# Kernel tuning notes

Hardware: AMD Instinct MI355X
Metric: run time of the kernel (lower is better)

## Reference

```python
import jax, jax.numpy as jnp
import numpy as np
from jax import lax

B, T, QD, ED, AD = 256, 512, 1024, 512, 128
NF, KS = 32, 31  # location filters, kernel size
PAD = (KS - 1) // 2


def setup_inputs() -> dict:
    key = jax.random.key(0)
    ks = jax.random.split(key, 12)
    query = jax.random.normal(ks[0], (B, QD), jnp.float32)
    inputs = jax.random.normal(ks[1], (B, T, ED), jnp.float32)
    processed_inputs = jax.random.normal(ks[2], (B, T, AD), jnp.float32)
    mask = jnp.ones((B, T), jnp.bool_)
    # init_states()
    attention_weights = jnp.zeros((B, T), jnp.float32)
    attention_weights_cum = jnp.zeros((B, T), jnp.float32)
    alpha = jnp.concatenate([jnp.ones((B, 1)), jnp.full((B, T - 1), 1e-7)], axis=1).astype(jnp.float32)
    u = 0.5 * jnp.ones((B, 1), jnp.float32)
    # parameters (xavier-ish scale)
    Wq = jax.random.normal(ks[3], (QD, AD), jnp.float32) * 0.03
    conv_w = jax.random.normal(ks[4], (NF, 2, KS), jnp.float32) * 0.1  # OIH
    Wloc = jax.random.normal(ks[5], (NF, AD), jnp.float32) * 0.1
    v_w = jax.random.normal(ks[6], (AD, 1), jnp.float32) * 0.1
    v_b = jnp.zeros((1,), jnp.float32)
    ta_w = jax.random.normal(ks[7], (ED + QD, 1), jnp.float32) * 0.02
    ta_b = jnp.zeros((1,), jnp.float32)
    return dict(query=query, inputs=inputs, processed_inputs=processed_inputs, mask=mask,
                attention_weights=attention_weights, attention_weights_cum=attention_weights_cum,
                alpha=alpha, u=u, Wq=Wq, conv_w=conv_w, Wloc=Wloc, v_w=v_w, v_b=v_b,
                ta_w=ta_w, ta_b=ta_b)


def reference(query, inputs, processed_inputs, mask, attention_weights,
              attention_weights_cum, alpha, u, Wq, conv_w, Wloc, v_w, v_b, ta_w, ta_b):
    # location-sensitive energies
    att_cat = jnp.stack([attention_weights, attention_weights_cum], axis=1)  # [B,2,T]
    loc = lax.conv_general_dilated(att_cat, conv_w, (1,), [(PAD, PAD)],
                                   dimension_numbers=('NCH', 'OIH', 'NCH'))  # [B,NF,T]
    proc_attn = jnp.einsum('bft,fa->bta', loc, Wloc)                         # [B,T,AD]
    proc_query = (query @ Wq)[:, None, :]                                    # [B,1,AD]
    energies = (jnp.tanh(proc_query + proc_attn + processed_inputs) @ v_w + v_b)[..., 0]  # [B,T]
    energies = jnp.where(mask, energies, -jnp.inf)
    alignment = jax.nn.softmax(energies, axis=-1)
    # forward attention recursion (training mode, no forward_attn_mask)
    shifted = jnp.pad(alpha[:, :-1], ((0, 0), (1, 0)))
    alpha_new = ((1.0 - u) * alpha + u * shifted + 1e-8) * alignment
    alpha_new = alpha_new / jnp.sum(alpha_new, axis=1, keepdims=True)
    context = jnp.einsum('bt,btd->bd', alpha_new, inputs)                    # [B,ED]
    # transition agent (state update; computed for faithfulness)
    u_new = jax.nn.sigmoid(jnp.concatenate([context, query], axis=-1) @ ta_w + ta_b)
    del u_new
    return context
```

## Files before the change

kernel.cpp:

```cpp
#include <hip/hip_runtime.h>

#define BB 256
#define TT 512
#define QD 1024
#define ED 512
#define AD 128
#define NF 32
#define KS 31
#define PADL 15
#define TCHUNK 256

typedef float f32x4 __attribute__((ext_vector_type(4)));

__device__ __forceinline__ float tanh_fast(float x) {
    float ex = __expf(2.0f * x);
    return 1.0f - 2.0f / (ex + 1.0f);
}

__global__ __launch_bounds__(256) void k_pq(const float* __restrict__ query,
                                            const float* __restrict__ Wq,
                                            float* __restrict__ pq) {
    int b = blockIdx.x;
    int tid = threadIdx.x;
    __shared__ float qs[QD];
    __shared__ float part[256];
    for (int i = tid; i < QD; i += 256) qs[i] = query[(size_t)b * QD + i];
    __syncthreads();
    int half = tid >> 7;
    int a = tid & 127;
    int kbase = half * 512;
    const float* wp = Wq + (size_t)kbase * AD + a;
    float acc = 0.f;
#pragma unroll 8
    for (int k = 0; k < 512; ++k)
        acc = fmaf(qs[kbase + k], wp[(size_t)k * AD], acc);
    part[tid] = acc;
    __syncthreads();
    if (tid < 128) pq[(size_t)b * AD + tid] = part[tid] + part[tid + 128];
}

__global__ __launch_bounds__(256) void k_energies(
    const float* __restrict__ attW, const float* __restrict__ attC,
    const float* __restrict__ convw, const float* __restrict__ Wloc,
    const float* __restrict__ pq, const float* __restrict__ pin,
    const float* __restrict__ vw, const float* __restrict__ vb,
    float* __restrict__ energies) {
    int b = blockIdx.x;
    int t0 = blockIdx.y * TCHUNK;
    int tid = threadIdx.x;

    __shared__ float sA[TCHUNK + 2 * PADL];
    __shared__ float sC[TCHUNK + 2 * PADL];
    __shared__ float sLoc[TCHUNK * 36];

    for (int i = tid; i < TCHUNK + 2 * PADL; i += 256) {
        int t = t0 + i - PADL;
        float a = 0.f, c = 0.f;
        if (t >= 0 && t < TT) {
            a = attW[(size_t)b * TT + t];
            c = attC[(size_t)b * TT + t];
        }
        sA[i] = a;
        sC[i] = c;
    }
    __syncthreads();

    {
        float winA[KS], winC[KS];
#pragma unroll
        for (int k = 0; k < KS; ++k) {
            winA[k] = sA[tid + k];
            winC[k] = sC[tid + k];
        }
        float* lrow = sLoc + tid * 36;
        for (int f = 0; f < NF; ++f) {
            const float* cwa = convw + f * (2 * KS);
            float acc = 0.f;
#pragma unroll
            for (int k = 0; k < KS; ++k) {
                acc = fmaf(cwa[k], winA[k], acc);
                acc = fmaf(cwa[KS + k], winC[k], acc);
            }
            lrow[f] = acc;
        }
    }
    __syncthreads();

    int wid = tid >> 6, lane = tid & 63;
    float2 w2[NF];
#pragma unroll
    for (int f = 0; f < NF; ++f)
        w2[f] = ((const float2*)(Wloc + f * AD))[lane];
    float2 pq2 = ((const float2*)(pq + (size_t)b * AD))[lane];
    float2 vw2 = ((const float2*)vw)[lane];
    float vbv = vb[0];

    for (int tt = wid; tt < TCHUNK; tt += 4) {
        int t = t0 + tt;
        const float4* lr = (const float4*)(sLoc + tt * 36);
        float pa0 = 0.f, pa1 = 0.f;
#pragma unroll
        for (int j = 0; j < 8; ++j) {
            float4 Lv = lr[j];
            pa0 = fmaf(Lv.x, w2[4 * j + 0].x, pa0);
            pa1 = fmaf(Lv.x, w2[4 * j + 0].y, pa1);
            pa0 = fmaf(Lv.y, w2[4 * j + 1].x, pa0);
            pa1 = fmaf(Lv.y, w2[4 * j + 1].y, pa1);
            pa0 = fmaf(Lv.z, w2[4 * j + 2].x, pa0);
            pa1 = fmaf(Lv.z, w2[4 * j + 2].y, pa1);
            pa0 = fmaf(Lv.w, w2[4 * j + 3].x, pa0);
            pa1 = fmaf(Lv.w, w2[4 * j + 3].y, pa1);
        }
        float2 p2 = ((const float2*)pin)[(size_t)(b * TT + t) * (AD / 2) + lane];
        float x0 = pq2.x + pa0 + p2.x;
        float x1 = pq2.y + pa1 + p2.y;
        float e = tanh_fast(x0) * vw2.x + tanh_fast(x1) * vw2.y;
#pragma unroll
        for (int off = 32; off > 0; off >>= 1)
            e += __shfl_xor(e, off, 64);
        if (lane == 0) energies[(size_t)b * TT + t] = e + vbv;
    }
}

__global__ __launch_bounds__(1024) void k_alpha_ctx(
    const float* __restrict__ energies, const float* __restrict__ alpha,
    const float* __restrict__ uArr, const float* __restrict__ inputs,
    float* __restrict__ out) {
    int b = blockIdx.x;
    int tid = threadIdx.x;
    int lane = tid & 63, wid = tid >> 6;

    __shared__ float al[TT];
    __shared__ float red[16];
    __shared__ f32x4 sacc[8][128];

    size_t base = (size_t)b * TT;
    float e = -1e30f, a0 = 0.f, ap = 0.f;
    if (tid < TT) {
        e = energies[base + tid];
        a0 = alpha[base + tid];
        ap = (tid == 0) ? 0.f : alpha[base + tid - 1];
    }
    float m = e;
#pragma unroll
    for (int off = 32; off > 0; off >>= 1) m = fmaxf(m, __shfl_xor(m, off, 64));
    if (lane == 0) red[wid] = m;
    __syncthreads();
    m = red[0];
#pragma unroll
    for (int i = 1; i < 16; ++i) m = fmaxf(m, red[i]);

    float u = uArr[b];
    float q = 0.f;
    if (tid < TT)
        q = fmaf(1.f - u, a0, u * ap + 1e-8f) * __expf(e - m);
    float s = q;
#pragma unroll
    for (int off = 32; off > 0; off >>= 1) s += __shfl_xor(s, off, 64);
    __syncthreads();
    if (lane == 0) red[wid] = s;
    __syncthreads();
    s = 0.f;
#pragma unroll
    for (int i = 0; i < 16; ++i) s += red[i];
    if (tid < TT) al[tid] = q / s;
    __syncthreads();

    int g = tid >> 7;
    int c = tid & 127;
    const f32x4* in4 = (const f32x4*)inputs;
    size_t rb = ((size_t)b * TT + (size_t)g * 64) * (ED / 4) + c;
    f32x4 acc = (f32x4)(0.f);
#pragma unroll 8
    for (int j = 0; j < 64; ++j) {
        f32x4 v = __builtin_nontemporal_load(&in4[rb + (size_t)j * (ED / 4)]);
        float w = al[g * 64 + j];
        acc.x = fmaf(w, v.x, acc.x);
        acc.y = fmaf(w, v.y, acc.y);
        acc.z = fmaf(w, v.z, acc.z);
        acc.w = fmaf(w, v.w, acc.w);
    }
    sacc[g][c] = acc;
    __syncthreads();
    if (tid < 128) {
        f32x4 t = sacc[0][tid];
#pragma unroll
        for (int i = 1; i < 8; ++i) t += sacc[i][tid];
        ((f32x4*)out)[(size_t)b * (ED / 4) + tid] = t;
    }
}

extern "C" void kernel_launch(void* const* d_in, const int* in_sizes, int n_in,
                              void* d_out, int out_size, void* d_ws, size_t ws_size,
                              hipStream_t stream) {
    (void)in_sizes; (void)n_in; (void)out_size; (void)ws_size;
    const float* query = (const float*)d_in[0];
    const float* inputs = (const float*)d_in[1];
    const float* pin   = (const float*)d_in[2];
    const float* attW  = (const float*)d_in[4];
    const float* attC  = (const float*)d_in[5];
    const float* alpha = (const float*)d_in[6];
    const float* uArr  = (const float*)d_in[7];
    const float* Wq    = (const float*)d_in[8];
    const float* convw = (const float*)d_in[9];
    const float* Wloc  = (const float*)d_in[10];
    const float* vw    = (const float*)d_in[11];
    const float* vb    = (const float*)d_in[12];

    float* ws = (float*)d_ws;
    float* pq       = ws;
    float* energies = pq + BB * AD;

    k_pq<<<dim3(BB), dim3(256), 0, stream>>>(query, Wq, pq);
    k_energies<<<dim3(BB, TT / TCHUNK), dim3(256), 0, stream>>>(
        attW, attC, convw, Wloc, pq, pin, vw, vb, energies);
    k_alpha_ctx<<<dim3(BB), dim3(1024), 0, stream>>>(
        energies, alpha, uArr, inputs, (float*)d_out);
}
```

Measured before the change: 124.5 us.

## Fuse energies, softmax weighting and context into T-chunked kernel with split reduction

Merges the energy computation with the forward-attention weighting and the context accumulation, so each (batch, T-chunk) block computes unnormalized weights and a partial context. A small follow-up kernel sums the partials and divides by the summed weights. This removes the energies round trip through global memory and spreads the large inputs read over more blocks (TCHUNK lowered to 128). It also splits the conv filters across two thread halves. Softmax no longer subtracts the max, which relies on the energies staying bounded (tanh output times v_w) to avoid exp overflow.

```diff
diff --git a/kernel.cpp b/kernel.cpp
--- a/kernel.cpp
+++ b/kernel.cpp
@@ -8,7 +8,8 @@
 #define NF 32
 #define KS 31
 #define PADL 15
-#define TCHUNK 256
+#define TCHUNK 128
+#define NCH (TT / TCHUNK)
 
 typedef float f32x4 __attribute__((ext_vector_type(4)));
 
@@ -39,19 +40,27 @@
     if (tid < 128) pq[(size_t)b * AD + tid] = part[tid] + part[tid + 128];
 }
 
-__global__ __launch_bounds__(256) void k_energies(
+__global__ __launch_bounds__(256) void k_fused(
     const float* __restrict__ attW, const float* __restrict__ attC,
     const float* __restrict__ convw, const float* __restrict__ Wloc,
     const float* __restrict__ pq, const float* __restrict__ pin,
     const float* __restrict__ vw, const float* __restrict__ vb,
-    float* __restrict__ energies) {
+    const float* __restrict__ alpha, const float* __restrict__ uArr,
+    const float* __restrict__ inputs,
+    float* __restrict__ partial, float* __restrict__ spart) {
     int b = blockIdx.x;
-    int t0 = blockIdx.y * TCHUNK;
+    int ch = blockIdx.y;
+    int t0 = ch * TCHUNK;
     int tid = threadIdx.x;
+    int wid = tid >> 6, lane = tid & 63;
 
     __shared__ float sA[TCHUNK + 2 * PADL];
     __shared__ float sC[TCHUNK + 2 * PADL];
+    __shared__ float sAl[TCHUNK + 1];
     __shared__ float sLoc[TCHUNK * 36];
+    __shared__ float sq[TCHUNK];
+    __shared__ float red[2];
+    __shared__ f32x4 sacc[2][128];
 
     for (int i = tid; i < TCHUNK + 2 * PADL; i += 256) {
         int t = t0 + i - PADL;
@@ -63,131 +72,123 @@
         sA[i] = a;
         sC[i] = c;
     }
+    if (tid < TCHUNK + 1) {
+        int t = t0 + tid - 1;
+        sAl[tid] = (t >= 0) ? alpha[(size_t)b * TT + t] : 0.f;
+    }
     __syncthreads();
 
     {
+        int tl = tid & 127, h = tid >> 7;
         float winA[KS], winC[KS];
 #pragma unroll
         for (int k = 0; k < KS; ++k) {
-            winA[k] = sA[tid + k];
-            winC[k] = sC[tid + k];
-        }
-        float* lrow = sLoc + tid * 36;
-        for (int f = 0; f < NF; ++f) {
-            const float* cwa = convw + f * (2 * KS);
+            winA[k] = sA[tl + k];
+            winC[k] = sC[tl + k];
+        }
+        float* lrow = sLoc + tl * 36 + h * 16;
+        const float* cw0 = convw + (h * 16) * (2 * KS);
+        for (int ff = 0; ff < 16; ++ff) {
+            const float* cwa = cw0 + ff * (2 * KS);
             float acc = 0.f;
 #pragma unroll
             for (int k = 0; k < KS; ++k) {
                 acc = fmaf(cwa[k], winA[k], acc);
                 acc = fmaf(cwa[KS + k], winC[k], acc);
             }
-            lrow[f] = acc;
-        }
-    }
-    __syncthreads();
-
-    int wid = tid >> 6, lane = tid & 63;
-    float2 w2[NF];
-#pragma unroll
-    for (int f = 0; f < NF; ++f)
-        w2[f] = ((const float2*)(Wloc + f * AD))[lane];
-    float2 pq2 = ((const float2*)(pq + (size_t)b * AD))[lane];
-    float2 vw2 = ((const float2*)vw)[lane];
-    float vbv = vb[0];
-
-    for (int tt = wid; tt < TCHUNK; tt += 4) {
-        int t = t0 + tt;
-        const float4* lr = (const float4*)(sLoc + tt * 36);
-        float pa0 = 0.f, pa1 = 0.f;
-#pragma unroll
-        for (int j = 0; j < 8; ++j) {
-            float4 Lv = lr[j];
-            pa0 = fmaf(Lv.x, w2[4 * j + 0].x, pa0);
-            pa1 = fmaf(Lv.x, w2[4 * j + 0].y, pa1);
-            pa0 = fmaf(Lv.y, w2[4 * j + 1].x, pa0);
-            pa1 = fmaf(Lv.y, w2[4 * j + 1].y, pa1);
-            pa0 = fmaf(Lv.z, w2[4 * j + 2].x, pa0);
-            pa1 = fmaf(Lv.z, w2[4 * j + 2].y, pa1);
-            pa0 = fmaf(Lv.w, w2[4 * j + 3].x, pa0);
-            pa1 = fmaf(Lv.w, w2[4 * j + 3].y, pa1);
-        }
-        float2 p2 = ((const float2*)pin)[(size_t)(b * TT + t) * (AD / 2) + lane];
-        float x0 = pq2.x + pa0 + p2.x;
-        float x1 = pq2.y + pa1 + p2.y;
-        float e = tanh_fast(x0) * vw2.x + tanh_fast(x1) * vw2.y;
-#pragma unroll
-        for (int off = 32; off > 0; off >>= 1)
-            e += __shfl_xor(e, off, 64);
-        if (lane == 0) energies[(size_t)b * TT + t] = e + vbv;
-    }
-}
-
-__global__ __launch_bounds__(1024) void k_alpha_ctx(
-    const float* __restrict__ energies, const float* __restrict__ alpha,
-    const float* __restrict__ uArr, const float* __restrict__ inputs,
+            lrow[ff] = acc;
+        }
+    }
+    __syncthreads();
+
+    {
+        float2 w2[NF];
+#pragma unroll
+        for (int f = 0; f < NF; ++f)
+            w2[f] = ((const float2*)(Wloc + f * AD))[lane];
+        float2 pq2 = ((const float2*)(pq + (size_t)b * AD))[lane];
+        float2 vw2 = ((const float2*)vw)[lane];
+        float vbv = vb[0];
+        float u = uArr[b];
+
+        for (int tt = wid; tt < TCHUNK; tt += 4) {
+            int t = t0 + tt;
+            const float4* lr = (const float4*)(sLoc + tt * 36);
+            float pa0 = 0.f, pa1 = 0.f;
+#pragma unroll
+            for (int j = 0; j < 8; ++j) {
+                float4 Lv = lr[j];
+                pa0 = fmaf(Lv.x, w2[4 * j + 0].x, pa0);
+                pa1 = fmaf(Lv.x, w2[4 * j + 0].y, pa1);
+                pa0 = fmaf(Lv.y, w2[4 * j + 1].x, pa0);
+                pa1 = fmaf(Lv.y, w2[4 * j + 1].y, pa1);
+                pa0 = fmaf(Lv.z, w2[4 * j + 2].x, pa0);
+                pa1 = fmaf(Lv.z, w2[4 * j + 2].y, pa1);
+                pa0 = fmaf(Lv.w, w2[4 * j + 3].x, pa0);
+                pa1 = fmaf(Lv.w, w2[4 * j + 3].y, pa1);
+            }
+            float2 p2 = ((const float2*)pin)[(size_t)(b * TT + t) * (AD / 2) + lane];
+            float x0 = pq2.x + pa0 + p2.x;
+            float x1 = pq2.y + pa1 + p2.y;
+            float e = tanh_fast(x0) * vw2.x + tanh_fast(x1) * vw2.y;
+#pragma unroll
+            for (int off = 32; off > 0; off >>= 1)
+                e += __shfl_xor(e, off, 64);
+            if (lane == 0) {
+                float w = fmaf(1.f - u, sAl[tt + 1], u * sAl[tt] + 1e-8f);
+                sq[tt] = w * __expf(e + vbv);
+            }
+        }
+    }
+    __syncthreads();
+
+    if (tid < TCHUNK) {
+        float v = sq[tid];
+#pragma unroll
+        for (int off = 32; off > 0; off >>= 1) v += __shfl_xor(v, off, 64);
+        if (lane == 0) red[wid] = v;
+    }
+
+    {
+        int g = tid >> 7, c = tid & 127;
+        const f32x4* in4 = (const f32x4*)inputs;
+        size_t rb = ((size_t)b * TT + t0 + g * 64) * (ED / 4) + c;
+        f32x4 acc = (f32x4)(0.f);
+#pragma unroll 8
+        for (int j = 0; j < 64; ++j) {
+            f32x4 v = __builtin_nontemporal_load(&in4[rb + (size_t)j * (ED / 4)]);
+            float w = sq[g * 64 + j];
+            acc.x = fmaf(w, v.x, acc.x);
+            acc.y = fmaf(w, v.y, acc.y);
+            acc.z = fmaf(w, v.z, acc.z);
+            acc.w = fmaf(w, v.w, acc.w);
+        }
+        sacc[g][c] = acc;
+    }
+    __syncthreads();
+    if (tid == 0) spart[(size_t)b * NCH + ch] = red[0] + red[1];
+    if (tid < 128) {
+        f32x4 t = sacc[0][tid] + sacc[1][tid];
+        ((f32x4*)partial)[((size_t)(b * NCH + ch)) * (ED / 4) + tid] = t;
+    }
+}
+
+__global__ __launch_bounds__(256) void k_reduce(
+    const float* __restrict__ partial, const float* __restrict__ spart,
     float* __restrict__ out) {
-    int b = blockIdx.x;
-    int tid = threadIdx.x;
-    int lane = tid & 63, wid = tid >> 6;
-
-    __shared__ float al[TT];
-    __shared__ float red[16];
-    __shared__ f32x4 sacc[8][128];
-
-    size_t base = (size_t)b * TT;
-    float e = -1e30f, a0 = 0.f, ap = 0.f;
-    if (tid < TT) {
-        e = energies[base + tid];
-        a0 = alpha[base + tid];
-        ap = (tid == 0) ? 0.f : alpha[base + tid - 1];
-    }
-    float m = e;
-#pragma unroll
-    for (int off = 32; off > 0; off >>= 1) m = fmaxf(m, __shfl_xor(m, off, 64));
-    if (lane == 0) red[wid] = m;
-    __syncthreads();
-    m = red[0];
-#pragma unroll
-    for (int i = 1; i < 16; ++i) m = fmaxf(m, red[i]);
-
-    float u = uArr[b];
-    float q = 0.f;
-    if (tid < TT)
-        q = fmaf(1.f - u, a0, u * ap + 1e-8f) * __expf(e - m);
-    float s = q;
-#pragma unroll
-    for (int off = 32; off > 0; off >>= 1) s += __shfl_xor(s, off, 64);
-    __syncthreads();
-    if (lane == 0) red[wid] = s;
-    __syncthreads();
-    s = 0.f;
-#pragma unroll
-    for (int i = 0; i < 16; ++i) s += red[i];
-    if (tid < TT) al[tid] = q / s;
-    __syncthreads();
-
-    int g = tid >> 7;
-    int c = tid & 127;
-    const f32x4* in4 = (const f32x4*)inputs;
-    size_t rb = ((size_t)b * TT + (size_t)g * 64) * (ED / 4) + c;
+    int idx = blockIdx.x * 256 + threadIdx.x;
+    int b = idx >> 7, c = idx & 127;
+    float s = 0.f;
+#pragma unroll
+    for (int j = 0; j < NCH; ++j) s += spart[(size_t)b * NCH + j];
+    const f32x4* p4 = (const f32x4*)partial;
     f32x4 acc = (f32x4)(0.f);
-#pragma unroll 8
-    for (int j = 0; j < 64; ++j) {
-        f32x4 v = __builtin_nontemporal_load(&in4[rb + (size_t)j * (ED / 4)]);
-        float w = al[g * 64 + j];
-        acc.x = fmaf(w, v.x, acc.x);
-        acc.y = fmaf(w, v.y, acc.y);
-        acc.z = fmaf(w, v.z, acc.z);
-        acc.w = fmaf(w, v.w, acc.w);
-    }
-    sacc[g][c] = acc;
-    __syncthreads();
-    if (tid < 128) {
-        f32x4 t = sacc[0][tid];
-#pragma unroll
-        for (int i = 1; i < 8; ++i) t += sacc[i][tid];
-        ((f32x4*)out)[(size_t)b * (ED / 4) + tid] = t;
-    }
+#pragma unroll
+    for (int j = 0; j < NCH; ++j)
+        acc += p4[((size_t)(b * NCH + j)) * (ED / 4) + c];
+    float inv = 1.f / s;
+    acc.x *= inv; acc.y *= inv; acc.z *= inv; acc.w *= inv;
+    ((f32x4*)out)[idx] = acc;
 }
 
 extern "C" void kernel_launch(void* const* d_in, const int* in_sizes, int n_in,
@@ -208,12 +209,14 @@
     const float* vb    = (const float*)d_in[12];
 
     float* ws = (float*)d_ws;
-    float* pq       = ws;
-    float* energies = pq + BB * AD;
+    float* pq      = ws;
+    float* partial = pq + BB * AD;
+    float* spart   = partial + BB * NCH * ED;
 
     k_pq<<<dim3(BB), dim3(256), 0, stream>>>(query, Wq, pq);
-    k_energies<<<dim3(BB, TT / TCHUNK), dim3(256), 0, stream>>>(
-        attW, attC, convw, Wloc, pq, pin, vw, vb, energies);
-    k_alpha_ctx<<<dim3(BB), dim3(1024), 0, stream>>>(
-        energies, alpha, uArr, inputs, (float*)d_out);
-}
+    k_fused<<<dim3(BB, NCH), dim3(256), 0, stream>>>(
+        attW, attC, convw, Wloc, pq, pin, vw, vb, alpha, uArr, inputs,
+        partial, spart);
+    k_reduce<<<dim3((BB * ED / 4) / 256), dim3(256), 0, stream>>>(
+        partial, spart, (float*)d_out);
+}
```

Result: slower. 132.6 us (+6.5%).

## Fuse alpha recursion into energies kernel and defer softmax normalization to context output

Applied to the files above, without the earlier changes.

The energies kernel now applies the forward-attention weighting ((1-u)*alpha + u*shifted alpha + eps) and exp directly, and writes unnormalized weights. The context kernel no longer computes the max and normalization before the weighted sum. It only sums the weights and scales the final context by the reciprocal. Wave reductions use DPP plus readlane instead of shuffles, and the context loop unroll goes from 8 to 16. Dropping the max subtraction relies on energies staying bounded (tanh output times v_w) to avoid exp overflow.

```diff
diff --git a/kernel.cpp b/kernel.cpp
--- a/kernel.cpp
+++ b/kernel.cpp
@@ -17,6 +17,35 @@
     return 1.0f - 2.0f / (ex + 1.0f);
 }
 
+__device__ __forceinline__ float dpp_xor1(float x) {
+    int y = __builtin_amdgcn_update_dpp(0, __float_as_int(x), 0xB1, 0xF, 0xF, true);
+    return x + __int_as_float(y);
+}
+__device__ __forceinline__ float dpp_xor2(float x) {
+    int y = __builtin_amdgcn_update_dpp(0, __float_as_int(x), 0x4E, 0xF, 0xF, true);
+    return x + __int_as_float(y);
+}
+__device__ __forceinline__ float dpp_xor4(float x) {
+    int y = __builtin_amdgcn_update_dpp(0, __float_as_int(x), 0x141, 0xF, 0xF, true);
+    return x + __int_as_float(y);
+}
+__device__ __forceinline__ float dpp_xor8(float x) {
+    int y = __builtin_amdgcn_update_dpp(0, __float_as_int(x), 0x140, 0xF, 0xF, true);
+    return x + __int_as_float(y);
+}
+__device__ __forceinline__ float wave_sum64(float x) {
+    x = dpp_xor1(x);
+    x = dpp_xor2(x);
+    x = dpp_xor4(x);
+    x = dpp_xor8(x);
+    int xi = __float_as_int(x);
+    float r0  = __int_as_float(__builtin_amdgcn_readlane(xi, 0));
+    float r16 = __int_as_float(__builtin_amdgcn_readlane(xi, 16));
+    float r32 = __int_as_float(__builtin_amdgcn_readlane(xi, 32));
+    float r48 = __int_as_float(__builtin_amdgcn_readlane(xi, 48));
+    return (r0 + r16) + (r32 + r48);
+}
+
 __global__ __launch_bounds__(256) void k_pq(const float* __restrict__ query,
                                             const float* __restrict__ Wq,
                                             float* __restrict__ pq) {
@@ -44,13 +73,15 @@
     const float* __restrict__ convw, const float* __restrict__ Wloc,
     const float* __restrict__ pq, const float* __restrict__ pin,
     const float* __restrict__ vw, const float* __restrict__ vb,
-    float* __restrict__ energies) {
+    const float* __restrict__ alpha, const float* __restrict__ uArr,
+    float* __restrict__ qOut) {
     int b = blockIdx.x;
     int t0 = blockIdx.y * TCHUNK;
     int tid = threadIdx.x;
 
     __shared__ float sA[TCHUNK + 2 * PADL];
     __shared__ float sC[TCHUNK + 2 * PADL];
+    __shared__ float sAl[TCHUNK + 1];
     __shared__ float sLoc[TCHUNK * 36];
 
     for (int i = tid; i < TCHUNK + 2 * PADL; i += 256) {
@@ -63,6 +94,10 @@
         sA[i] = a;
         sC[i] = c;
     }
+    for (int i = tid; i < TCHUNK + 1; i += 256) {
+        int t = t0 + i - 1;
+        sAl[i] = (t >= 0) ? alpha[(size_t)b * TT + t] : 0.f;
+    }
     __syncthreads();
 
     {
@@ -94,6 +129,7 @@
     float2 pq2 = ((const float2*)(pq + (size_t)b * AD))[lane];
     float2 vw2 = ((const float2*)vw)[lane];
     float vbv = vb[0];
+    float u = uArr[b];
 
     for (int tt = wid; tt < TCHUNK; tt += 4) {
         int t = t0 + tt;
@@ -114,17 +150,17 @@
         float2 p2 = ((const float2*)pin)[(size_t)(b * TT + t) * (AD / 2) + lane];
         float x0 = pq2.x + pa0 + p2.x;
         float x1 = pq2.y + pa1 + p2.y;
-        float e = tanh_fast(x0) * vw2.x + tanh_fast(x1) * vw2.y;
-#pragma unroll
-        for (int off = 32; off > 0; off >>= 1)
-            e += __shfl_xor(e, off, 64);
-        if (lane == 0) energies[(size_t)b * TT + t] = e + vbv;
-    }
-}
-
-__global__ __launch_bounds__(1024) void k_alpha_ctx(
-    const float* __restrict__ energies, const float* __restrict__ alpha,
-    const float* __restrict__ uArr, const float* __restrict__ inputs,
+        float epart = tanh_fast(x0) * vw2.x + tanh_fast(x1) * vw2.y;
+        float e = wave_sum64(epart);
+        if (lane == 0) {
+            float w = fmaf(1.f - u, sAl[tt + 1], u * sAl[tt] + 1e-8f);
+            qOut[(size_t)b * TT + t] = w * __expf(e + vbv);
+        }
+    }
+}
+
+__global__ __launch_bounds__(1024) void k_ctx(
+    const float* __restrict__ qIn, const float* __restrict__ inputs,
     float* __restrict__ out) {
     int b = blockIdx.x;
     int tid = threadIdx.x;
@@ -135,43 +171,24 @@
     __shared__ f32x4 sacc[8][128];
 
     size_t base = (size_t)b * TT;
-    float e = -1e30f, a0 = 0.f, ap = 0.f;
+    float q = 0.f;
     if (tid < TT) {
-        e = energies[base + tid];
-        a0 = alpha[base + tid];
-        ap = (tid == 0) ? 0.f : alpha[base + tid - 1];
-    }
-    float m = e;
-#pragma unroll
-    for (int off = 32; off > 0; off >>= 1) m = fmaxf(m, __shfl_xor(m, off, 64));
-    if (lane == 0) red[wid] = m;
-    __syncthreads();
-    m = red[0];
-#pragma unroll
-    for (int i = 1; i < 16; ++i) m = fmaxf(m, red[i]);
-
-    float u = uArr[b];
-    float q = 0.f;
-    if (tid < TT)
-        q = fmaf(1.f - u, a0, u * ap + 1e-8f) * __expf(e - m);
-    float s = q;
-#pragma unroll
-    for (int off = 32; off > 0; off >>= 1) s += __shfl_xor(s, off, 64);
-    __syncthreads();
+        q = qIn[base + tid];
+        al[tid] = q;
+    }
+    float s = wave_sum64(q);
     if (lane == 0) red[wid] = s;
     __syncthreads();
     s = 0.f;
 #pragma unroll
     for (int i = 0; i < 16; ++i) s += red[i];
-    if (tid < TT) al[tid] = q / s;
-    __syncthreads();
 
     int g = tid >> 7;
     int c = tid & 127;
     const f32x4* in4 = (const f32x4*)inputs;
     size_t rb = ((size_t)b * TT + (size_t)g * 64) * (ED / 4) + c;
     f32x4 acc = (f32x4)(0.f);
-#pragma unroll 8
+#pragma unroll 16
     for (int j = 0; j < 64; ++j) {
         f32x4 v = __builtin_nontemporal_load(&in4[rb + (size_t)j * (ED / 4)]);
         float w = al[g * 64 + j];
@@ -186,6 +203,8 @@
         f32x4 t = sacc[0][tid];
 #pragma unroll
         for (int i = 1; i < 8; ++i) t += sacc[i][tid];
+        float inv = 1.f / s;
+        t.x *= inv; t.y *= inv; t.z *= inv; t.w *= inv;
         ((f32x4*)out)[(size_t)b * (ED / 4) + tid] = t;
     }
 }
@@ -208,12 +227,11 @@
     const float* vb    = (const float*)d_in[12];
 
     float* ws = (float*)d_ws;
-    float* pq       = ws;
-    float* energies = pq + BB * AD;
+    float* pq   = ws;
+    float* qBuf = pq + BB * AD;
 
     k_pq<<<dim3(BB), dim3(256), 0, stream>>>(query, Wq, pq);
     k_energies<<<dim3(BB, TT / TCHUNK), dim3(256), 0, stream>>>(
-        attW, attC, convw, Wloc, pq, pin, vw, vb, energies);
-    k_alpha_ctx<<<dim3(BB), dim3(1024), 0, stream>>>(
-        energies, alpha, uArr, inputs, (float*)d_out);
-}
+        attW, attC, convw, Wloc, pq, pin, vw, vb, alpha, uArr, qBuf);
+    k_ctx<<<dim3(BB), dim3(1024), 0, stream>>>(qBuf, inputs, (float*)d_out);
+}
```

After: 120.4 us. 1.03x faster.
